# Kernel tuning notes

Measured on AMD Instinct MI355X. Metric: run time of the kernel, lower is better.

## Reference

```python
import jax, jax.numpy as jnp
from jax import lax
import numpy as np

B, L, H = 2048, 2048, 64
DP_DIM, EPS_DIM = 4, 1
IN_DIM = DP_DIM + EPS_DIM + 1  # 6, per docstring


def setup_inputs() -> dict:
    key = jax.random.key(0)
    ks = jax.random.split(key, 13)
    s = 1.0 / np.sqrt(H)
    u = lambda k, shape: jax.random.uniform(k, shape, jnp.float32, -s, s)
    return {
        "dP": jax.random.normal(ks[0], (B, L, DP_DIM), jnp.float32),
        "eps": jax.random.normal(ks[1], (B, L, EPS_DIM), jnp.float32),
        "W_ih0": u(ks[2], (4 * H, IN_DIM)), "W_hh0": u(ks[3], (4 * H, H)),
        "b_ih0": u(ks[4], (4 * H,)), "b_hh0": u(ks[5], (4 * H,)),
        "W_ih1": u(ks[6], (4 * H, H)), "W_hh1": u(ks[7], (4 * H, H)),
        "b_ih1": u(ks[8], (4 * H,)), "b_hh1": u(ks[9], (4 * H,)),
        "W_head": u(ks[10], (1, H)), "b_head": u(ks[11], (1,)),
        "lengths": jax.random.randint(ks[12], (B,), 1, L + 1),
        "reverse": 0,
    }


def _lstm_cell(x, h, c, W_ih, W_hh, b_ih, b_hh):
    # PyTorch LSTMCell gate layout: i, f, g, o
    g = x @ W_ih.T + b_ih + h @ W_hh.T + b_hh
    i, f, gg, o = jnp.split(g, 4, axis=-1)
    c_new = jax.nn.sigmoid(f) * c + jax.nn.sigmoid(i) * jnp.tanh(gg)
    h_new = jax.nn.sigmoid(o) * jnp.tanh(c_new)
    return h_new, c_new


def _forward(dP, eps, W_ih0, W_hh0, b_ih0, b_hh0, W_ih1, W_hh1, b_ih1, b_hh1,
             W_head, b_head, lengths, reverse):
    Bsz, Ln, _ = dP.shape
    Hd = W_hh0.shape[1]
    x_all = jnp.concatenate([dP, eps], axis=-1).transpose(1, 0, 2)  # (L,B,5)
    t_vals = jnp.arange(Ln)
    if reverse:
        x_all = x_all[::-1]
        t_vals = t_vals[::-1]

    h_d0 = jnp.zeros((Bsz, 1), dP.dtype)
    hs0 = jnp.zeros((2, Bsz, Hd), dP.dtype)
    cs0 = jnp.zeros((2, Bsz, Hd), dP.dtype)

    def step(carry, inp):
        h_d, hs, cs = carry
        x5, t = inp
        active = (t < lengths)[:, None]  # (B,1) bool
        x = jnp.concatenate([x5, h_d], axis=-1)  # (B,6)
        h0, c0 = _lstm_cell(x, hs[0], cs[0], W_ih0, W_hh0, b_ih0, b_hh0)
        h1, c1 = _lstm_cell(h0, hs[1], cs[1], W_ih1, W_hh1, b_ih1, b_hh1)
        delta = h1 @ W_head.T + b_head  # (B,1)
        h_prev = h_d
        h_d_new = jnp.where(active, h_d + delta, h_d)
        # inactive rows have their LSTM state zeroed (matches torch.where(..., zero))
        new_hs = jnp.where(active[None], jnp.stack([h0, h1]), jnp.zeros_like(hs))
        new_cs = jnp.where(active[None], jnp.stack([c0, c1]), jnp.zeros_like(cs))
        return (h_d_new, new_hs, new_cs), (h_prev, delta)

    _, (h_seq, d_seq) = lax.scan(step, (h_d0, hs0, cs0), (x_all, t_vals))
    h_seq = h_seq.transpose(1, 0, 2)  # (B,L,1) in iteration order
    d_seq = d_seq.transpose(1, 0, 2)
    if reverse:
        h_seq = h_seq[:, ::-1]
        d_seq = d_seq[:, ::-1]
    return h_seq, d_seq


def reference(dP, eps, W_ih0, W_hh0, b_ih0, b_hh0, W_ih1, W_hh1, b_ih1, b_hh1,
              W_head, b_head, lengths, reverse):
    return _forward(dP, eps, W_ih0, W_hh0, b_ih0, b_hh0, W_ih1, W_hh1,
                    b_ih1, b_hh1, W_head, b_head, lengths, reverse)
```

## Files before the change

### kernel.cpp

```cpp
#include <hip/hip_runtime.h>
#include <hip/hip_bf16.h>

#define B_TOT 2048
#define L_SEQ 2048
#define NBLK  256
#define BQ    8
#define NWAVE 8
#define XBS   328

typedef __attribute__((ext_vector_type(8))) short bf16x8;
typedef __attribute__((ext_vector_type(4))) float f32x4;

#if __has_builtin(__builtin_amdgcn_exp2f)
static __device__ __forceinline__ float fexp2(float x){ return __builtin_amdgcn_exp2f(x); }
#else
static __device__ __forceinline__ float fexp2(float x){ return exp2f(x); }
#endif
#if __has_builtin(__builtin_amdgcn_rcpf)
static __device__ __forceinline__ float frcp (float x){ return __builtin_amdgcn_rcpf(x); }
#else
static __device__ __forceinline__ float frcp (float x){ return 1.0f / x; }
#endif

static __device__ __forceinline__ unsigned short f2bf(float f){
  union { float f; unsigned int u; } v; v.f = f;
  unsigned int u = v.u;
  u += 0x7FFFu + ((u >> 16) & 1u);
  return (unsigned short)(u >> 16);
}

static __device__ __forceinline__ float sigm_pre(float x, float bpre){
  return frcp(1.f + fexp2(__builtin_fmaf(x, -1.4426950408889634f, bpre)));
}
static __device__ __forceinline__ float tanh_pre(float x, float bpre){
  return 1.f - 2.f*frcp(1.f + fexp2(__builtin_fmaf(x, 2.8853900817779268f, bpre)));
}
static __device__ __forceinline__ float cell_act(float gi,float gf,float gg,float go,
    float bi,float bf,float bg,float bo, float& c, bool act){
  float is = sigm_pre(gi, bi);
  float fs = sigm_pre(gf, bf);
  float gt = tanh_pre(gg, bg);
  float os = sigm_pre(go, bo);
  float cn = __builtin_fmaf(fs, c, is*gt);
  float h  = os * tanh_pre(cn, 0.f);
  c = act ? cn : 0.f;
  return h;
}
static __device__ __forceinline__ bf16x8 maskz(bf16x8 v, bool keep){
  union { bf16x8 v; unsigned int u[4]; } x; x.v = v;
  unsigned int m = keep ? 0xFFFFFFFFu : 0u;
  x.u[0]&=m; x.u[1]&=m; x.u[2]&=m; x.u[3]&=m;
  return x.v;
}

__global__ __launch_bounds__(512, 2)
void dh_lstm(const float* __restrict__ dP, const float* __restrict__ eps,
             const float* __restrict__ Wih0, const float* __restrict__ Whh0,
             const float* __restrict__ bih0, const float* __restrict__ bhh0,
             const float* __restrict__ Wih1, const float* __restrict__ Whh1,
             const float* __restrict__ bih1, const float* __restrict__ bhh1,
             const float* __restrict__ Whead, const float* __restrict__ bhead_p,
             const int* __restrict__ lengths, const int* __restrict__ revp,
             float* __restrict__ out)
{
  __shared__ unsigned short XB[16][XBS];
  __shared__ float dpart[NWAVE][16];

  const int tid = threadIdx.x;
  const int l   = tid & 63;
  const int w   = tid >> 6;
  const int g   = l >> 4;
  const int r16 = l & 15;
  const int b0  = blockIdx.x * BQ;
  const int rev = revp[0];

  {
    unsigned int* p = (unsigned int*)&XB[0][0];
    for (int i = tid; i < 16*XBS/2; i += 512) p[i] = 0u;
    if (tid < NWAVE*16) ((float*)dpart)[tid] = 0.f;
  }

  bf16x8 A0[2][3], A1[2][4];
  {
    const int u  = r16 >> 1;
    const int t0 = r16 & 1;
#pragma unroll
    for (int tau = 0; tau < 2; ++tau){
      const int j = 64*(2*tau + t0) + 8*w + u;
#pragma unroll
      for (int k = 0; k < 3; ++k){
        bf16x8 a;
#pragma unroll
        for (int e = 0; e < 8; ++e){
          const int c = 32*k + 8*g + e;
          float v = 0.f;
          if (c < 64) v = Whh0[j*64 + c];
          else if (c < 70) v = Wih0[j*6 + (c-64)];
          a[e] = (short)f2bf(v);
        }
        A0[tau][k] = a;
      }
#pragma unroll
      for (int k = 0; k < 4; ++k){
        bf16x8 a;
#pragma unroll
        for (int e = 0; e < 8; ++e){
          const int c = 32*k + 8*g + e;
          const float v = (c < 64) ? Wih1[j*64 + c] : Whh1[j*64 + (c-64)];
          a[e] = (short)f2bf(v);
        }
        A1[tau][k] = a;
      }
    }
  }

  float bp0[4][2], bp1[4][2], wx[4][2];
#pragma unroll
  for (int t4 = 0; t4 < 4; ++t4){
#pragma unroll
    for (int j = 0; j < 2; ++j){
      const int jj = 64*t4 + 8*w + 2*g + j;
      const float sc = (t4 == 2) ? 2.8853900817779268f : -1.4426950408889634f;
      bp0[t4][j] = sc * (bih0[jj] + bhh0[jj]);
      bp1[t4][j] = sc * (bih1[jj] + bhh1[jj]);
      wx[t4][j]  = Wih0[jj*6 + 5];
    }
  }
  const float wh0 = Whead[8*w + 2*g + 0];
  const float wh1 = Whead[8*w + 2*g + 1];
  const float bhead = bhead_p[0];
  const int   lenb  = lengths[b0 + (r16 & 7)];

  __syncthreads();

  float xr0=0,xr1=0,xr2=0,xr3=0,xr4=0;
  const bool xload = (w == 1) && (l < 8);
  if (xload){
    const int t0p = rev ? (L_SEQ-1) : 0;
    const float4 v = *(const float4*)(dP + ((size_t)(b0+l)*L_SEQ + t0p)*4);
    const float ev = eps[(size_t)(b0+l)*L_SEQ + t0p];
    unsigned int* dst = (unsigned int*)&XB[l][256];
    dst[0] = (unsigned int)f2bf(v.x) | ((unsigned int)f2bf(v.y) << 16);
    dst[1] = (unsigned int)f2bf(v.z) | ((unsigned int)f2bf(v.w) << 16);
    XB[l][256+4] = f2bf(ev);
    const int t1p = rev ? (L_SEQ-2) : 1;
    const float4 v1 = *(const float4*)(dP + ((size_t)(b0+l)*L_SEQ + t1p)*4);
    xr0=v1.x; xr1=v1.y; xr2=v1.z; xr3=v1.w;
    xr4 = eps[(size_t)(b0+l)*L_SEQ + t1p];
  }
  __syncthreads();

  float c00=0,c01=0,c10=0,c11=0, h_d=0;
  const unsigned short* Brow = &XB[r16][0];

  for (int t = 0; t < L_SEQ; ++t){
    const int par = t & 1;
    const int tp  = rev ? (L_SEQ-1-t) : t;
    const bool act = tp < lenb;
    const bool ap  = (t == 0) || ((rev ? (L_SEQ - t) : (t-1)) < lenb);

    f32x4 acc0a={0,0,0,0}, acc0b={0,0,0,0}, acc1a={0,0,0,0}, acc1b={0,0,0,0};
    {
      const int hb  = 64*(par^1);
      const int h1b = 128 + 64*(par^1);
      bf16x8 bk0 = *(const bf16x8*)(Brow + hb + 8*g);
      bf16x8 bk1 = *(const bf16x8*)(Brow + hb + 32 + 8*g);
      bf16x8 bx  = *(const bf16x8*)(Brow + 256 + 32*par + 8*g);
      bf16x8 bh2 = *(const bf16x8*)(Brow + h1b + 8*g);
      bf16x8 bh3 = *(const bf16x8*)(Brow + h1b + 32 + 8*g);
      bk0 = maskz(bk0, ap); bk1 = maskz(bk1, ap);
      bh2 = maskz(bh2, ap); bh3 = maskz(bh3, ap);
      acc0a = __builtin_amdgcn_mfma_f32_16x16x32_bf16(A0[0][0], bk0, acc0a,0,0,0);
      acc0b = __builtin_amdgcn_mfma_f32_16x16x32_bf16(A0[1][0], bk0, acc0b,0,0,0);
      acc0a = __builtin_amdgcn_mfma_f32_16x16x32_bf16(A0[0][1], bk1, acc0a,0,0,0);
      acc0b = __builtin_amdgcn_mfma_f32_16x16x32_bf16(A0[1][1], bk1, acc0b,0,0,0);
      acc0a = __builtin_amdgcn_mfma_f32_16x16x32_bf16(A0[0][2], bx,  acc0a,0,0,0);
      acc0b = __builtin_amdgcn_mfma_f32_16x16x32_bf16(A0[1][2], bx,  acc0b,0,0,0);
      acc1a = __builtin_amdgcn_mfma_f32_16x16x32_bf16(A1[0][2], bh2, acc1a,0,0,0);
      acc1b = __builtin_amdgcn_mfma_f32_16x16x32_bf16(A1[1][2], bh2, acc1b,0,0,0);
      acc1a = __builtin_amdgcn_mfma_f32_16x16x32_bf16(A1[0][3], bh3, acc1a,0,0,0);
      acc1b = __builtin_amdgcn_mfma_f32_16x16x32_bf16(A1[1][3], bh3, acc1b,0,0,0);
    }
    {
      float h0 = cell_act(__builtin_fmaf(wx[0][0],h_d,acc0a[0]),
                          __builtin_fmaf(wx[1][0],h_d,acc0a[1]),
                          __builtin_fmaf(wx[2][0],h_d,acc0b[0]),
                          __builtin_fmaf(wx[3][0],h_d,acc0b[1]),
                          bp0[0][0],bp0[1][0],bp0[2][0],bp0[3][0], c00, act);
      float h1 = cell_act(__builtin_fmaf(wx[0][1],h_d,acc0a[2]),
                          __builtin_fmaf(wx[1][1],h_d,acc0a[3]),
                          __builtin_fmaf(wx[2][1],h_d,acc0b[2]),
                          __builtin_fmaf(wx[3][1],h_d,acc0b[3]),
                          bp0[0][1],bp0[1][1],bp0[2][1],bp0[3][1], c01, act);
      *(unsigned int*)&XB[r16][64*par + 8*w + 2*g] =
        (unsigned int)f2bf(h0) | ((unsigned int)f2bf(h1) << 16);
      if (xload){
        unsigned int* dst = (unsigned int*)&XB[l][256 + 32*(par^1)];
        dst[0] = (unsigned int)f2bf(xr0) | ((unsigned int)f2bf(xr1) << 16);
        dst[1] = (unsigned int)f2bf(xr2) | ((unsigned int)f2bf(xr3) << 16);
        XB[l][256 + 32*(par^1) + 4] = f2bf(xr4);
        int ts = t + 2;
        int tpn = rev ? (L_SEQ-1-ts) : ts;
        tpn = tpn < 0 ? 0 : (tpn >= L_SEQ ? L_SEQ-1 : tpn);
        const float4 v = *(const float4*)(dP + ((size_t)(b0+l)*L_SEQ + tpn)*4);
        xr0=v.x; xr1=v.y; xr2=v.z; xr3=v.w;
        xr4 = eps[(size_t)(b0+l)*L_SEQ + tpn];
      }
    }
    __syncthreads();
    {
      const int h0b = 64*par;
      bf16x8 bk0 = *(const bf16x8*)(Brow + h0b + 8*g);
      bf16x8 bk1 = *(const bf16x8*)(Brow + h0b + 32 + 8*g);
      acc1a = __builtin_amdgcn_mfma_f32_16x16x32_bf16(A1[0][0], bk0, acc1a,0,0,0);
      acc1b = __builtin_amdgcn_mfma_f32_16x16x32_bf16(A1[1][0], bk0, acc1b,0,0,0);
      acc1a = __builtin_amdgcn_mfma_f32_16x16x32_bf16(A1[0][1], bk1, acc1a,0,0,0);
      acc1b = __builtin_amdgcn_mfma_f32_16x16x32_bf16(A1[1][1], bk1, acc1b,0,0,0);
    }
    {
      float h0 = cell_act(acc1a[0],acc1a[1],acc1b[0],acc1b[1],
                          bp1[0][0],bp1[1][0],bp1[2][0],bp1[3][0], c10, act);
      float h1 = cell_act(acc1a[2],acc1a[3],acc1b[2],acc1b[3],
                          bp1[0][1],bp1[1][1],bp1[2][1],bp1[3][1], c11, act);
      *(unsigned int*)&XB[r16][128 + 64*par + 8*w + 2*g] =
        (unsigned int)f2bf(h0) | ((unsigned int)f2bf(h1) << 16);
      float s = __builtin_fmaf(wh0, h0, wh1*h1);
      s += __shfl_xor(s, 16, 64);
      s += __shfl_xor(s, 32, 64);
      if (l < 16) dpart[w][l] = s;
    }
    __syncthreads();
    {
      float dsum = bhead;
#pragma unroll
      for (int ww = 0; ww < NWAVE; ++ww) dsum += dpart[ww][r16];
      const float h_prev = h_d;
      if (act) h_d += dsum;
      if (w == 0 && l < 8){
        const int bi = b0 + l;
        out[(size_t)bi*L_SEQ + tp] = h_prev;
        out[(size_t)B_TOT*L_SEQ + (size_t)bi*L_SEQ + tp] = dsum;
      }
    }
  }
}

extern "C" void kernel_launch(void* const* d_in, const int* in_sizes, int n_in,
                              void* d_out, int out_size, void* d_ws, size_t ws_size,
                              hipStream_t stream) {
  (void)in_sizes; (void)n_in; (void)d_ws; (void)ws_size; (void)out_size;
  dh_lstm<<<dim3(NBLK), dim3(512), 0, stream>>>(
      (const float*)d_in[0],  (const float*)d_in[1],
      (const float*)d_in[2],  (const float*)d_in[3],
      (const float*)d_in[4],  (const float*)d_in[5],
      (const float*)d_in[6],  (const float*)d_in[7],
      (const float*)d_in[8],  (const float*)d_in[9],
      (const float*)d_in[10], (const float*)d_in[11],
      (const int*)d_in[12],   (const int*)d_in[13],
      (float*)d_out);
}
```

Before: 2.316 ms.

## Deduplicate padded-batch cell math via lane shuffles and masked h0 buffers

The MFMA tile has 16 batch columns but only 8 are real. The gate outputs are now redistributed with xor-8 shuffles so each lane evaluates one real cell instead of two, roughly halving the transcendental work. Per-step masking of the B operands is replaced by storing h0 twice, raw for layer 1 and masked for the next step's recurrence, and h1 is stored pre-masked. Packing uses v_cvt_pk_bf16_f32, the head reduction is rewritten with vectorised LDS reads, and launch bounds drop to one block per CU, which adds extra shuffles and LDS traffic.

```diff
diff --git a/kernel.cpp b/kernel.cpp
--- a/kernel.cpp
+++ b/kernel.cpp
@@ -6,7 +6,11 @@
 #define NBLK  256
 #define BQ    8
 #define NWAVE 8
-#define XBS   328
+#define XBS   454
+#define H0RAW 0
+#define H1M   128
+#define XOFF  256
+#define H0M   320
 
 typedef __attribute__((ext_vector_type(8))) short bf16x8;
 typedef __attribute__((ext_vector_type(4))) float f32x4;
@@ -28,6 +32,11 @@
   u += 0x7FFFu + ((u >> 16) & 1u);
   return (unsigned short)(u >> 16);
 }
+static __device__ __forceinline__ unsigned int cvtpk2(float a){
+  unsigned int r;
+  asm("v_cvt_pk_bf16_f32 %0, %1, %2" : "=v"(r) : "v"(a), "v"(a));
+  return r;
+}
 
 static __device__ __forceinline__ float sigm_pre(float x, float bpre){
   return frcp(1.f + fexp2(__builtin_fmaf(x, -1.4426950408889634f, bpre)));
@@ -46,14 +55,8 @@
   c = act ? cn : 0.f;
   return h;
 }
-static __device__ __forceinline__ bf16x8 maskz(bf16x8 v, bool keep){
-  union { bf16x8 v; unsigned int u[4]; } x; x.v = v;
-  unsigned int m = keep ? 0xFFFFFFFFu : 0u;
-  x.u[0]&=m; x.u[1]&=m; x.u[2]&=m; x.u[3]&=m;
-  return x.v;
-}
-
-__global__ __launch_bounds__(512, 2)
+
+__global__ __launch_bounds__(512, 1)
 void dh_lstm(const float* __restrict__ dP, const float* __restrict__ eps,
              const float* __restrict__ Wih0, const float* __restrict__ Whh0,
              const float* __restrict__ bih0, const float* __restrict__ bhh0,
@@ -64,20 +67,21 @@
              float* __restrict__ out)
 {
   __shared__ unsigned short XB[16][XBS];
-  __shared__ float dpart[NWAVE][16];
+  __shared__ float dpart2[8][8];
 
   const int tid = threadIdx.x;
   const int l   = tid & 63;
   const int w   = tid >> 6;
   const int g   = l >> 4;
   const int r16 = l & 15;
+  const int r8  = r16 & 7;
+  const int hb  = r16 >> 3;
   const int b0  = blockIdx.x * BQ;
   const int rev = revp[0];
 
   {
     unsigned int* p = (unsigned int*)&XB[0][0];
     for (int i = tid; i < 16*XBS/2; i += 512) p[i] = 0u;
-    if (tid < NWAVE*16) ((float*)dpart)[tid] = 0.f;
   }
 
   bf16x8 A0[2][3], A1[2][4];
@@ -114,22 +118,19 @@
     }
   }
 
-  float bp0[4][2], bp1[4][2], wx[4][2];
+  const int ju = 8*w + 2*g + hb;
+  float bp0v[4], bp1v[4], wxv[4];
 #pragma unroll
   for (int t4 = 0; t4 < 4; ++t4){
-#pragma unroll
-    for (int j = 0; j < 2; ++j){
-      const int jj = 64*t4 + 8*w + 2*g + j;
-      const float sc = (t4 == 2) ? 2.8853900817779268f : -1.4426950408889634f;
-      bp0[t4][j] = sc * (bih0[jj] + bhh0[jj]);
-      bp1[t4][j] = sc * (bih1[jj] + bhh1[jj]);
-      wx[t4][j]  = Wih0[jj*6 + 5];
-    }
-  }
-  const float wh0 = Whead[8*w + 2*g + 0];
-  const float wh1 = Whead[8*w + 2*g + 1];
+    const int jj = 64*t4 + ju;
+    const float sc = (t4 == 2) ? 2.8853900817779268f : -1.4426950408889634f;
+    bp0v[t4] = sc * (bih0[jj] + bhh0[jj]);
+    bp1v[t4] = sc * (bih1[jj] + bhh1[jj]);
+    wxv[t4]  = Wih0[jj*6 + 5];
+  }
+  const float wh    = Whead[ju];
   const float bhead = bhead_p[0];
-  const int   lenb  = lengths[b0 + (r16 & 7)];
+  const int   lenb  = lengths[b0 + r8];
 
   __syncthreads();
 
@@ -139,10 +140,10 @@
     const int t0p = rev ? (L_SEQ-1) : 0;
     const float4 v = *(const float4*)(dP + ((size_t)(b0+l)*L_SEQ + t0p)*4);
     const float ev = eps[(size_t)(b0+l)*L_SEQ + t0p];
-    unsigned int* dst = (unsigned int*)&XB[l][256];
+    unsigned int* dst = (unsigned int*)&XB[l][XOFF];
     dst[0] = (unsigned int)f2bf(v.x) | ((unsigned int)f2bf(v.y) << 16);
     dst[1] = (unsigned int)f2bf(v.z) | ((unsigned int)f2bf(v.w) << 16);
-    XB[l][256+4] = f2bf(ev);
+    XB[l][XOFF+4] = f2bf(ev);
     const int t1p = rev ? (L_SEQ-2) : 1;
     const float4 v1 = *(const float4*)(dP + ((size_t)(b0+l)*L_SEQ + t1p)*4);
     xr0=v1.x; xr1=v1.y; xr2=v1.z; xr3=v1.w;
@@ -150,26 +151,22 @@
   }
   __syncthreads();
 
-  float c00=0,c01=0,c10=0,c11=0, h_d=0;
+  float c0s=0.f, c1s=0.f, h_d=0.f;
   const unsigned short* Brow = &XB[r16][0];
 
   for (int t = 0; t < L_SEQ; ++t){
     const int par = t & 1;
     const int tp  = rev ? (L_SEQ-1-t) : t;
     const bool act = tp < lenb;
-    const bool ap  = (t == 0) || ((rev ? (L_SEQ - t) : (t-1)) < lenb);
 
     f32x4 acc0a={0,0,0,0}, acc0b={0,0,0,0}, acc1a={0,0,0,0}, acc1b={0,0,0,0};
     {
-      const int hb  = 64*(par^1);
-      const int h1b = 128 + 64*(par^1);
-      bf16x8 bk0 = *(const bf16x8*)(Brow + hb + 8*g);
-      bf16x8 bk1 = *(const bf16x8*)(Brow + hb + 32 + 8*g);
-      bf16x8 bx  = *(const bf16x8*)(Brow + 256 + 32*par + 8*g);
-      bf16x8 bh2 = *(const bf16x8*)(Brow + h1b + 8*g);
-      bf16x8 bh3 = *(const bf16x8*)(Brow + h1b + 32 + 8*g);
-      bk0 = maskz(bk0, ap); bk1 = maskz(bk1, ap);
-      bh2 = maskz(bh2, ap); bh3 = maskz(bh3, ap);
+      const int hbuf = 64*(par^1);
+      bf16x8 bk0 = *(const bf16x8*)(Brow + H0M + hbuf + 8*g);
+      bf16x8 bk1 = *(const bf16x8*)(Brow + H0M + hbuf + 32 + 8*g);
+      bf16x8 bx  = *(const bf16x8*)(Brow + XOFF + 32*par + 8*g);
+      bf16x8 bh2 = *(const bf16x8*)(Brow + H1M + hbuf + 8*g);
+      bf16x8 bh3 = *(const bf16x8*)(Brow + H1M + hbuf + 32 + 8*g);
       acc0a = __builtin_amdgcn_mfma_f32_16x16x32_bf16(A0[0][0], bk0, acc0a,0,0,0);
       acc0b = __builtin_amdgcn_mfma_f32_16x16x32_bf16(A0[1][0], bk0, acc0b,0,0,0);
       acc0a = __builtin_amdgcn_mfma_f32_16x16x32_bf16(A0[0][1], bk1, acc0a,0,0,0);
@@ -182,23 +179,28 @@
       acc1b = __builtin_amdgcn_mfma_f32_16x16x32_bf16(A1[1][3], bh3, acc1b,0,0,0);
     }
     {
-      float h0 = cell_act(__builtin_fmaf(wx[0][0],h_d,acc0a[0]),
-                          __builtin_fmaf(wx[1][0],h_d,acc0a[1]),
-                          __builtin_fmaf(wx[2][0],h_d,acc0b[0]),
-                          __builtin_fmaf(wx[3][0],h_d,acc0b[1]),
-                          bp0[0][0],bp0[1][0],bp0[2][0],bp0[3][0], c00, act);
-      float h1 = cell_act(__builtin_fmaf(wx[0][1],h_d,acc0a[2]),
-                          __builtin_fmaf(wx[1][1],h_d,acc0a[3]),
-                          __builtin_fmaf(wx[2][1],h_d,acc0b[2]),
-                          __builtin_fmaf(wx[3][1],h_d,acc0b[3]),
-                          bp0[0][1],bp0[1][1],bp0[2][1],bp0[3][1], c01, act);
-      *(unsigned int*)&XB[r16][64*par + 8*w + 2*g] =
-        (unsigned int)f2bf(h0) | ((unsigned int)f2bf(h1) << 16);
+      const float xi = __shfl_xor(acc0a[2], 8);
+      const float xf = __shfl_xor(acc0a[3], 8);
+      const float xg = __shfl_xor(acc0b[2], 8);
+      const float xo = __shfl_xor(acc0b[3], 8);
+      float gi = hb ? xi : acc0a[0];
+      float gf = hb ? xf : acc0a[1];
+      float gg = hb ? xg : acc0b[0];
+      float go = hb ? xo : acc0b[1];
+      gi = __builtin_fmaf(wxv[0], h_d, gi);
+      gf = __builtin_fmaf(wxv[1], h_d, gf);
+      gg = __builtin_fmaf(wxv[2], h_d, gg);
+      go = __builtin_fmaf(wxv[3], h_d, go);
+      const float h0v = cell_act(gi,gf,gg,go, bp0v[0],bp0v[1],bp0v[2],bp0v[3], c0s, act);
+      const unsigned int rr = cvtpk2(h0v);
+      const unsigned int rm = act ? rr : 0u;
+      XB[r8][H0RAW + 64*par + ju] = (unsigned short)rr;
+      XB[r8][H0M   + 64*par + ju] = (unsigned short)rm;
       if (xload){
-        unsigned int* dst = (unsigned int*)&XB[l][256 + 32*(par^1)];
+        unsigned int* dst = (unsigned int*)&XB[l][XOFF + 32*(par^1)];
         dst[0] = (unsigned int)f2bf(xr0) | ((unsigned int)f2bf(xr1) << 16);
         dst[1] = (unsigned int)f2bf(xr2) | ((unsigned int)f2bf(xr3) << 16);
-        XB[l][256 + 32*(par^1) + 4] = f2bf(xr4);
+        XB[l][XOFF + 32*(par^1) + 4] = f2bf(xr4);
         int ts = t + 2;
         int tpn = rev ? (L_SEQ-1-ts) : ts;
         tpn = tpn < 0 ? 0 : (tpn >= L_SEQ ? L_SEQ-1 : tpn);
@@ -209,31 +211,38 @@
     }
     __syncthreads();
     {
-      const int h0b = 64*par;
-      bf16x8 bk0 = *(const bf16x8*)(Brow + h0b + 8*g);
-      bf16x8 bk1 = *(const bf16x8*)(Brow + h0b + 32 + 8*g);
+      bf16x8 bk0 = *(const bf16x8*)(Brow + H0RAW + 64*par + 8*g);
+      bf16x8 bk1 = *(const bf16x8*)(Brow + H0RAW + 64*par + 32 + 8*g);
       acc1a = __builtin_amdgcn_mfma_f32_16x16x32_bf16(A1[0][0], bk0, acc1a,0,0,0);
       acc1b = __builtin_amdgcn_mfma_f32_16x16x32_bf16(A1[1][0], bk0, acc1b,0,0,0);
       acc1a = __builtin_amdgcn_mfma_f32_16x16x32_bf16(A1[0][1], bk1, acc1a,0,0,0);
       acc1b = __builtin_amdgcn_mfma_f32_16x16x32_bf16(A1[1][1], bk1, acc1b,0,0,0);
     }
     {
-      float h0 = cell_act(acc1a[0],acc1a[1],acc1b[0],acc1b[1],
-                          bp1[0][0],bp1[1][0],bp1[2][0],bp1[3][0], c10, act);
-      float h1 = cell_act(acc1a[2],acc1a[3],acc1b[2],acc1b[3],
-                          bp1[0][1],bp1[1][1],bp1[2][1],bp1[3][1], c11, act);
-      *(unsigned int*)&XB[r16][128 + 64*par + 8*w + 2*g] =
-        (unsigned int)f2bf(h0) | ((unsigned int)f2bf(h1) << 16);
-      float s = __builtin_fmaf(wh0, h0, wh1*h1);
-      s += __shfl_xor(s, 16, 64);
-      s += __shfl_xor(s, 32, 64);
-      if (l < 16) dpart[w][l] = s;
+      const float xi = __shfl_xor(acc1a[2], 8);
+      const float xf = __shfl_xor(acc1a[3], 8);
+      const float xg = __shfl_xor(acc1b[2], 8);
+      const float xo = __shfl_xor(acc1b[3], 8);
+      const float gi = hb ? xi : acc1a[0];
+      const float gf = hb ? xf : acc1a[1];
+      const float gg = hb ? xg : acc1b[0];
+      const float go = hb ? xo : acc1b[1];
+      const float h1v = cell_act(gi,gf,gg,go, bp1v[0],bp1v[1],bp1v[2],bp1v[3], c1s, act);
+      const unsigned int rr = cvtpk2(h1v);
+      const unsigned int rm = act ? rr : 0u;
+      XB[r8][H1M + 64*par + ju] = (unsigned short)rm;
+      float s = wh * h1v;
+      s += __shfl_xor(s, 8);
+      s += __shfl_xor(s, 16);
+      s += __shfl_xor(s, 32);
+      if (l < 8) dpart2[l][w] = s;
     }
     __syncthreads();
     {
-      float dsum = bhead;
-#pragma unroll
-      for (int ww = 0; ww < NWAVE; ++ww) dsum += dpart[ww][r16];
+      const f32x4 dp0 = *(const f32x4*)&dpart2[r8][0];
+      const f32x4 dp1 = *(const f32x4*)&dpart2[r8][4];
+      const float dsum = bhead + ((dp0[0]+dp0[1])+(dp0[2]+dp0[3]))
+                               + ((dp1[0]+dp1[1])+(dp1[2]+dp1[3]));
       const float h_prev = h_d;
       if (act) h_d += dsum;
       if (w == 0 && l < 8){
```

New measurement: 4.765 ms. +105.7%, slower.
